# Kernel optimization log

Measured on AMD Instinct MI355X. Metric: run time of the kernel, lower is better.

## Reference

```python
import jax, jax.numpy as jnp
import numpy as np

N_NODES = 100000
N_EDGES = 3200000
D_IN = 256
D_HID = 32
N_CLS = 40
K_HOPS = 3


def setup_inputs() -> dict:
    key = jax.random.key(0)
    ks = jax.random.split(key, 6)
    x = jax.random.normal(ks[0], (N_NODES, D_IN), dtype=jnp.float32)
    edge_index = jax.random.randint(ks[1], (2, N_EDGES), 0, N_NODES, dtype=jnp.int64)
    edge_attr = jax.random.uniform(ks[2], (N_EDGES, 1), dtype=jnp.float32)
    W_conv = jax.random.normal(ks[3], (D_HID, D_IN), dtype=jnp.float32) / np.sqrt(D_IN)
    b_conv = jnp.zeros((D_HID,), dtype=jnp.float32)
    W_fc = jax.random.normal(ks[4], (N_CLS, D_HID), dtype=jnp.float32) * np.sqrt(2.0 / D_HID)
    b_fc = jnp.zeros((N_CLS,), dtype=jnp.float32)
    return {"x": x, "edge_index": edge_index, "edge_attr": edge_attr,
            "W_conv": W_conv, "b_conv": b_conv, "W_fc": W_fc, "b_fc": b_fc}


def _gcn_norm(edge_index, edge_weight, num_nodes):
    # add self-loops with weight 1 (PyG gcn_norm default)
    loop = jnp.arange(num_nodes, dtype=edge_index.dtype)
    row = jnp.concatenate([edge_index[0], loop])
    col = jnp.concatenate([edge_index[1], loop])
    w = jnp.concatenate([edge_weight, jnp.ones((num_nodes,), edge_weight.dtype)])
    deg = jax.ops.segment_sum(w, col, num_segments=num_nodes)
    deg_inv_sqrt = jnp.where(deg > 0, jax.lax.rsqrt(deg), 0.0)
    norm = deg_inv_sqrt[row] * w * deg_inv_sqrt[col]
    return row, col, norm


def reference(x, edge_index, edge_attr, W_conv, b_conv, W_fc, b_fc):
    N = x.shape[0]
    row, col, norm = _gcn_norm(edge_index, edge_attr.squeeze(-1), N)
    # K-hop symmetric-normalized diffusion: x <- (D^-1/2 (A+I) D^-1/2) x
    h = x
    for _ in range(K_HOPS):
        h = jax.ops.segment_sum(norm[:, None] * h[row], col, num_segments=N)
    h = h @ W_conv.T + b_conv          # SGConv linear
    h = jax.nn.elu(h)
    h = h @ W_fc.T + b_fc              # classifier
    return jax.nn.log_softmax(h, axis=1)
```

## Files before the change

kernel.cpp:

```cpp
#include <hip/hip_runtime.h>
#include <math.h>

#define N_NODES 100000
#define N_EDGES 3200000
#define D_IN    256
#define D_HID   32
#define N_CLS   40

#define NPART  196
#define HROW   200
#define NB1    256
#define CHUNK1 12500
#define SUB    2500

typedef unsigned int u32;
typedef unsigned short u16;

__device__ __forceinline__ float bf2f(u16 v) {
    return __uint_as_float(((u32)v) << 16);
}
__device__ __forceinline__ u16 f2bf(float f) {
    u32 u = __float_as_uint(f);
    u32 r = u + 0x7FFFu + ((u >> 16) & 1u);
    return (u16)(r >> 16);
}


__global__ __launch_bounds__(256) void k_histA(const int* __restrict__ col,
                                               u32* __restrict__ histmat) {
    __shared__ u32 h[256];
    int t = threadIdx.x;
    h[t] = 0;
    __syncthreads();
    int s = blockIdx.x * CHUNK1;
    for (int i = s + t; i < s + CHUNK1; i += 256)
        atomicAdd(&h[((u32)col[i]) >> 9], 1u);
    __syncthreads();
    if (t < HROW) histmat[blockIdx.x * HROW + t] = (t < NPART) ? h[t] : 0u;
}


__global__ __launch_bounds__(256) void k_scanA(u32* __restrict__ histmat,
                                               int* __restrict__ cstart) {
    __shared__ u32 sc[256];
    int p = threadIdx.x;
    u32 run = 0;
    for (int b = 0; b < NB1; ++b) {
        u32 v = (p < NPART) ? histmat[b * HROW + p] : 0u;
        if (p < NPART) histmat[b * HROW + p] = run;
        run += v;
    }
    u32 own = (p < NPART) ? run : 0u;
    sc[p] = own;
    __syncthreads();
    for (int off = 1; off < 256; off <<= 1) {
        u32 v = (p >= off) ? sc[p - off] : 0u;
        __syncthreads();
        sc[p] += v;
        __syncthreads();
    }
    if (p < NPART) cstart[p] = (int)(sc[p] - own);
    if (p == NPART - 1) cstart[NPART] = (int)sc[p];
}


__global__ __launch_bounds__(256) void k_part(const int* __restrict__ row,
                                              const int* __restrict__ col,
                                              const float* __restrict__ w,
                                              const u32* __restrict__ histmat,
                                              const int* __restrict__ cstart,
                                              uint2* __restrict__ coarse) {
    __shared__ u32 shist[256], sscan[256], scur[256], gbase[256], rcur[256];
    __shared__ uint2 stage[SUB];
    __shared__ u32 gdst[SUB];
    int t = threadIdx.x;
    rcur[t] = (t < NPART) ? ((u32)cstart[t] + histmat[blockIdx.x * HROW + t]) : 0u;
    int s0 = blockIdx.x * CHUNK1;

    for (int sc_ = 0; sc_ < CHUNK1; sc_ += SUB) {
        int s = s0 + sc_;
        shist[t] = 0;
        __syncthreads();
        for (int i = s + t; i < s + SUB; i += 256)
            atomicAdd(&shist[((u32)col[i]) >> 9], 1u);
        __syncthreads();
        u32 own = shist[t];
        sscan[t] = own;
        __syncthreads();
        for (int off = 1; off < 256; off <<= 1) {
            u32 v = (t >= off) ? sscan[t - off] : 0u;
            __syncthreads();
            sscan[t] += v;
            __syncthreads();
        }
        u32 exc = sscan[t] - own;
        scur[t]  = exc;
        gbase[t] = rcur[t] - exc;
        __syncthreads();
        for (int i = s + t; i < s + SUB; i += 256) {
            u32 c = (u32)col[i];
            u32 pid = c >> 9;
            u32 pos = atomicAdd(&scur[pid], 1u);
            stage[pos] = make_uint2(((c & 511u) << 17) | (u32)row[i], __float_as_uint(w[i]));
            gdst[pos]  = gbase[pid] + pos;
        }
        __syncthreads();
        for (int i = t; i < SUB; i += 256) coarse[gdst[i]] = stage[i];
        rcur[t] += shist[t];
        __syncthreads();
    }
}


__global__ __launch_bounds__(256) void k_part2(const uint2* __restrict__ coarse,
                                               const int* __restrict__ cstart,
                                               float* __restrict__ dis,
                                               int* __restrict__ startp,
                                               u32* __restrict__ csr) {
    __shared__ float wsuml[512];
    __shared__ u32 cntl[512];
    __shared__ u32 curl[512];
    __shared__ u32 psum[256];
    int p = blockIdx.x, t = threadIdx.x;
    int s = cstart[p], e = cstart[p + 1];
    int nbase = p << 9;

    cntl[t] = 0; cntl[t + 256] = 0;
    wsuml[t] = 0.f; wsuml[t + 256] = 0.f;
    __syncthreads();
    for (int i = s + t; i < e; i += 256) {
        uint2 en = coarse[i];
        u32 l = en.x >> 17;
        atomicAdd(&cntl[l], 1u);
        atomicAdd(&wsuml[l], __uint_as_float(en.y));
    }
    __syncthreads();
    for (int l = t; l < 512; l += 256) {
        int node = nbase + l;
        if (node < N_NODES) dis[node] = rsqrtf(1.0f + wsuml[l]);
    }
    u32 a0 = cntl[2 * t], a1 = cntl[2 * t + 1];
    psum[t] = a0 + a1;
    __syncthreads();
    for (int off = 1; off < 256; off <<= 1) {
        u32 v = (t >= off) ? psum[t - off] : 0u;
        __syncthreads();
        psum[t] += v;
        __syncthreads();
    }
    u32 excl = psum[t] - (a0 + a1);
    u32 c0 = (u32)s + excl, c1 = c0 + a0;
    curl[2 * t] = c0; curl[2 * t + 1] = c1;
    int n0 = nbase + 2 * t, n1 = n0 + 1;
    if (n0 < N_NODES) startp[n0] = (int)c0;
    if (n1 < N_NODES) startp[n1] = (int)c1;
    if (p == NPART - 1 && t == 255) startp[N_NODES] = e;
    __syncthreads();
    for (int i = s + t; i < e; i += 256) {
        uint2 en = coarse[i];
        u32 l = en.x >> 17;
        u32 src = en.x & 0x1FFFFu;
        float wv = __uint_as_float(en.y);
        u32 q = (u32)(wv * 32768.0f + 0.5f);
        if (q > 32767u) q = 32767u;
        u32 pos = atomicAdd(&curl[l], 1u);
        csr[pos] = (src << 15) | q;
    }
}


#define LSTRIDE 260

__global__ __launch_bounds__(256) void k_gemm1(const float* __restrict__ x,
                                               const float* __restrict__ Wc,
                                               const float* __restrict__ dis,
                                               u16* __restrict__ g) {
    __shared__ float xs[32 * LSTRIDE];
    __shared__ float wsl[32 * LSTRIDE];
    const int tid  = threadIdx.x;
    const int base = blockIdx.x * 32;

    for (int i = tid; i < 2048; i += 256) {
        int r = i >> 6, j = i & 63;
        float4 v = reinterpret_cast<const float4*>(x)[(size_t)(base + r) * 64 + j];
        *reinterpret_cast<float4*>(&xs[r * LSTRIDE + j * 4]) = v;
    }
    for (int i = tid; i < 2048; i += 256) {
        int r = i >> 6, j = i & 63;
        float4 v = reinterpret_cast<const float4*>(Wc)[i];
        *reinterpret_cast<float4*>(&wsl[r * LSTRIDE + j * 4]) = v;
    }
    __syncthreads();

    const int node = tid >> 3;
    const int og   = tid & 7;
    float4 acc = make_float4(0.f, 0.f, 0.f, 0.f);
    const float* xrow = &xs[node * LSTRIDE];
    const float* w0 = &wsl[(og     ) * LSTRIDE];
    const float* w1 = &wsl[(og +  8) * LSTRIDE];
    const float* w2 = &wsl[(og + 16) * LSTRIDE];
    const float* w3 = &wsl[(og + 24) * LSTRIDE];

#pragma unroll 4
    for (int k = 0; k < 256; k += 4) {
        float4 xv = *reinterpret_cast<const float4*>(&xrow[k]);
        float4 a4 = *reinterpret_cast<const float4*>(&w0[k]);
        float4 b4 = *reinterpret_cast<const float4*>(&w1[k]);
        float4 c4 = *reinterpret_cast<const float4*>(&w2[k]);
        float4 d4 = *reinterpret_cast<const float4*>(&w3[k]);
        acc.x += xv.x * a4.x + xv.y * a4.y + xv.z * a4.z + xv.w * a4.w;
        acc.y += xv.x * b4.x + xv.y * b4.y + xv.z * b4.z + xv.w * b4.w;
        acc.z += xv.x * c4.x + xv.y * c4.y + xv.z * c4.z + xv.w * c4.w;
        acc.w += xv.x * d4.x + xv.y * d4.y + xv.z * d4.z + xv.w * d4.w;
    }
    float dv = dis[base + node];
    size_t gb = (size_t)(base + node) * D_HID;
    g[gb + og     ] = f2bf(acc.x * dv);
    g[gb + og +  8] = f2bf(acc.y * dv);
    g[gb + og + 16] = f2bf(acc.z * dv);
    g[gb + og + 24] = f2bf(acc.w * dv);
}


__global__ __launch_bounds__(256) void k_pull(const int* __restrict__ start,
                                              const u32* __restrict__ csr,
                                              const float* __restrict__ dis,
                                              const u16* __restrict__ h,
                                              u16* __restrict__ out,
                                              int sq) {
    int g    = blockIdx.x * 8 + (threadIdx.x >> 5);
    int lane = threadIdx.x & 31;
    if (g >= N_NODES) return;

    int s = start[g];
    int e = start[g + 1];
    float acc = bf2f(h[(size_t)g * D_HID + lane]);

    for (int base = s; base < e; base += 32) {
        int idx = base + lane;
        u32 p = (idx < e) ? csr[idx] : 0u;
        int rem = e - base;
        for (int jj = 0; jj < 32; jj += 8) {
            if (jj >= rem) break;
#pragma unroll
            for (int j = 0; j < 8; ++j) {
                u32 pj = __shfl(p, jj + j, 32);
                float nv = (float)(pj & 32767u) * (1.0f / 32768.0f);
                u32 src = pj >> 15;
                acc += nv * bf2f(h[(size_t)src * D_HID + lane]);
            }
        }
    }
    float sc = dis[g];
    if (sq) sc *= sc;
    out[(size_t)g * D_HID + lane] = f2bf(sc * acc);
}


__global__ __launch_bounds__(256) void k_final(const u16* __restrict__ h,
                                               const float* __restrict__ bc,
                                               const float* __restrict__ Wfc,
                                               const float* __restrict__ bf,
                                               float* __restrict__ out) {
    __shared__ float wf[N_CLS * D_HID];
    __shared__ float bcs[D_HID];
    __shared__ float bfs[N_CLS];
    const int tid = threadIdx.x;
    for (int i = tid; i < N_CLS * D_HID; i += 256) wf[i] = Wfc[i];
    if (tid < D_HID) bcs[tid] = bc[tid];
    if (tid < N_CLS) bfs[tid] = bf[tid];
    __syncthreads();

    int node = blockIdx.x * 256 + tid;
    if (node >= N_NODES) return;

    float a[D_HID];
    const u32* hp = reinterpret_cast<const u32*>(h + (size_t)node * D_HID);
#pragma unroll
    for (int j = 0; j < 16; ++j) {
        u32 v = hp[j];
        float z0 = bf2f((u16)(v & 0xFFFFu)) + bcs[j * 2 + 0];
        float z1 = bf2f((u16)(v >> 16))     + bcs[j * 2 + 1];
        a[j * 2 + 0] = z0 > 0.f ? z0 : expm1f(z0);
        a[j * 2 + 1] = z1 > 0.f ? z1 : expm1f(z1);
    }

    float logits[N_CLS];
    float m = -1e30f;
#pragma unroll
    for (int c = 0; c < N_CLS; ++c) {
        float accv = bfs[c];
        const float* wr = &wf[c * D_HID];
#pragma unroll
        for (int o = 0; o < D_HID; ++o) accv += a[o] * wr[o];
        logits[c] = accv;
        m = fmaxf(m, accv);
    }
    float sum = 0.f;
#pragma unroll
    for (int c = 0; c < N_CLS; ++c) sum += expf(logits[c] - m);
    float lse = m + logf(sum);
    float* op = out + (size_t)node * N_CLS;
#pragma unroll
    for (int c = 0; c < N_CLS; ++c) op[c] = logits[c] - lse;
}


extern "C" void kernel_launch(void* const* d_in, const int* in_sizes, int n_in,
                              void* d_out, int out_size, void* d_ws, size_t ws_size,
                              hipStream_t stream) {
    const float* x   = (const float*)d_in[0];
    const int*   ei  = (const int*)d_in[1];
    const float* ea  = (const float*)d_in[2];
    const float* Wc  = (const float*)d_in[3];
    const float* bc  = (const float*)d_in[4];
    const float* Wfc = (const float*)d_in[5];
    const float* bf  = (const float*)d_in[6];
    float* out = (float*)d_out;
    float* ws  = (float*)d_ws;

    const int* row = ei;
    const int* col = ei + N_EDGES;

    float* dis     = ws;
    int*   cstart  = (int*)(ws + 100000);
    u32*   histmat = (u32*)(ws + 100224);
    int*   startp  = (int*)(ws + 151424);
    uint2* coarse  = (uint2*)(ws + 251428);
    u32*   csr     = (u32*)(ws + 6651428);
    u16*   bufA    = (u16*)(ws + 251428);
    u16*   bufB    = (u16*)(ws + 1851428);

    const int GN = (N_NODES + 255) / 256;
    const int GP = (N_NODES + 7) / 8;

    k_histA <<<NB1, 256, 0, stream>>>(col, histmat);
    k_scanA <<<1, 256, 0, stream>>>(histmat, cstart);
    k_part  <<<NB1, 256, 0, stream>>>(row, col, ea, histmat, cstart, coarse);
    k_part2 <<<NPART, 256, 0, stream>>>(coarse, cstart, dis, startp, csr);

    k_gemm1 <<<N_NODES / 32, 256, 0, stream>>>(x, Wc, dis, bufA);

    k_pull  <<<GP, 256, 0, stream>>>(startp, csr, dis, bufA, bufB, 1);
    k_pull  <<<GP, 256, 0, stream>>>(startp, csr, dis, bufB, bufA, 1);
    k_pull  <<<GP, 256, 0, stream>>>(startp, csr, dis, bufA, bufB, 0);

    k_final <<<GN, 256, 0, stream>>>(bufB, bc, Wfc, bf, out);
}
```

Baseline: 565.0 us.

## Use bf16 dot2 in projection GEMM and full-wavefront edge pulls

The projection GEMM now converts x and W to packed bf16 in shared memory, uses bf16 dot2 instructions, and computes two nodes per thread over 64-node blocks, which halves LDS traffic and raises reuse of the W loads. The pull kernel gives each node a full 64-lane wavefront: the two half-waves process alternate edges and their sums are combined with a cross-half shuffle, so the 32-wide wave32-style mapping no longer leaves half of each wave idle. The trade-offs are extra bf16 rounding of the inputs and fewer nodes handled per block in the pull kernel.

```diff
diff --git a/kernel.cpp b/kernel.cpp
--- a/kernel.cpp
+++ b/kernel.cpp
@@ -23,6 +23,30 @@
     u32 u = __float_as_uint(f);
     u32 r = u + 0x7FFFu + ((u >> 16) & 1u);
     return (u16)(r >> 16);
+}
+__device__ __forceinline__ u32 pack2bf(float lo, float hi) {
+    return (u32)f2bf(lo) | ((u32)f2bf(hi) << 16);
+}
+
+#if defined(__has_builtin)
+#if __has_builtin(__builtin_amdgcn_fdot2_f32_bf16)
+#define HAVE_DOT2 1
+#endif
+#endif
+
+#ifdef HAVE_DOT2
+typedef __bf16 bf16x2 __attribute__((ext_vector_type(2)));
+#endif
+
+__device__ __forceinline__ float dot2bf(u32 a, u32 b, float c) {
+#ifdef HAVE_DOT2
+    return __builtin_amdgcn_fdot2_f32_bf16(__builtin_bit_cast(bf16x2, a),
+                                           __builtin_bit_cast(bf16x2, b), c, false);
+#else
+    float al = __uint_as_float(a << 16), ah = __uint_as_float(a & 0xFFFF0000u);
+    float bl = __uint_as_float(b << 16), bh = __uint_as_float(b & 0xFFFF0000u);
+    return c + al * bl + ah * bh;
+#endif
 }
 
 
@@ -169,56 +193,77 @@
 }
 
 
-#define LSTRIDE 260
+#define XST 130
 
 __global__ __launch_bounds__(256) void k_gemm1(const float* __restrict__ x,
                                                const float* __restrict__ Wc,
                                                const float* __restrict__ dis,
                                                u16* __restrict__ g) {
-    __shared__ float xs[32 * LSTRIDE];
-    __shared__ float wsl[32 * LSTRIDE];
+    __shared__ u32 xs[64 * XST];
+    __shared__ u32 wsl[32 * XST];
     const int tid  = threadIdx.x;
-    const int base = blockIdx.x * 32;
-
-    for (int i = tid; i < 2048; i += 256) {
-        int r = i >> 6, j = i & 63;
-        float4 v = reinterpret_cast<const float4*>(x)[(size_t)(base + r) * 64 + j];
-        *reinterpret_cast<float4*>(&xs[r * LSTRIDE + j * 4]) = v;
-    }
-    for (int i = tid; i < 2048; i += 256) {
-        int r = i >> 6, j = i & 63;
-        float4 v = reinterpret_cast<const float4*>(Wc)[i];
-        *reinterpret_cast<float4*>(&wsl[r * LSTRIDE + j * 4]) = v;
-    }
-    __syncthreads();
-
-    const int node = tid >> 3;
-    const int og   = tid & 7;
-    float4 acc = make_float4(0.f, 0.f, 0.f, 0.f);
-    const float* xrow = &xs[node * LSTRIDE];
-    const float* w0 = &wsl[(og     ) * LSTRIDE];
-    const float* w1 = &wsl[(og +  8) * LSTRIDE];
-    const float* w2 = &wsl[(og + 16) * LSTRIDE];
-    const float* w3 = &wsl[(og + 24) * LSTRIDE];
+    const int base = blockIdx.x * 64;
+    const int nrows = (N_NODES - base) < 64 ? (N_NODES - base) : 64;
+
+    for (int i = tid; i < 4096; i += 256) {
+        int r = i >> 7, kk = i & 127;
+        float2 v = reinterpret_cast<const float2*>(Wc)[i];
+        wsl[r * XST + kk] = pack2bf(v.x, v.y);
+    }
+    for (int i = tid; i < nrows * 128; i += 256) {
+        int r = i >> 7, kk = i & 127;
+        float2 v = reinterpret_cast<const float2*>(x)[(size_t)(base + r) * 128 + kk];
+        xs[r * XST + kk] = pack2bf(v.x, v.y);
+    }
+    __syncthreads();
+
+    const int np = tid >> 3;
+    const int og = tid & 7;
+    if (2 * np >= nrows) return;
+
+    const u32* x0 = &xs[(2 * np    ) * XST];
+    const u32* x1 = &xs[(2 * np + 1) * XST];
+    const u32* w0 = &wsl[(og     ) * XST];
+    const u32* w1 = &wsl[(og +  8) * XST];
+    const u32* w2 = &wsl[(og + 16) * XST];
+    const u32* w3 = &wsl[(og + 24) * XST];
+
+    float a00 = 0.f, a01 = 0.f, a02 = 0.f, a03 = 0.f;
+    float a10 = 0.f, a11 = 0.f, a12 = 0.f, a13 = 0.f;
 
 #pragma unroll 4
-    for (int k = 0; k < 256; k += 4) {
-        float4 xv = *reinterpret_cast<const float4*>(&xrow[k]);
-        float4 a4 = *reinterpret_cast<const float4*>(&w0[k]);
-        float4 b4 = *reinterpret_cast<const float4*>(&w1[k]);
-        float4 c4 = *reinterpret_cast<const float4*>(&w2[k]);
-        float4 d4 = *reinterpret_cast<const float4*>(&w3[k]);
-        acc.x += xv.x * a4.x + xv.y * a4.y + xv.z * a4.z + xv.w * a4.w;
-        acc.y += xv.x * b4.x + xv.y * b4.y + xv.z * b4.z + xv.w * b4.w;
-        acc.z += xv.x * c4.x + xv.y * c4.y + xv.z * c4.z + xv.w * c4.w;
-        acc.w += xv.x * d4.x + xv.y * d4.y + xv.z * d4.z + xv.w * d4.w;
-    }
-    float dv = dis[base + node];
-    size_t gb = (size_t)(base + node) * D_HID;
-    g[gb + og     ] = f2bf(acc.x * dv);
-    g[gb + og +  8] = f2bf(acc.y * dv);
-    g[gb + og + 16] = f2bf(acc.z * dv);
-    g[gb + og + 24] = f2bf(acc.w * dv);
+    for (int kk = 0; kk < 128; kk += 2) {
+        uint2 X0 = *reinterpret_cast<const uint2*>(&x0[kk]);
+        uint2 X1 = *reinterpret_cast<const uint2*>(&x1[kk]);
+        uint2 W0 = *reinterpret_cast<const uint2*>(&w0[kk]);
+        uint2 W1 = *reinterpret_cast<const uint2*>(&w1[kk]);
+        uint2 W2 = *reinterpret_cast<const uint2*>(&w2[kk]);
+        uint2 W3 = *reinterpret_cast<const uint2*>(&w3[kk]);
+        a00 = dot2bf(X0.x, W0.x, a00); a00 = dot2bf(X0.y, W0.y, a00);
+        a01 = dot2bf(X0.x, W1.x, a01); a01 = dot2bf(X0.y, W1.y, a01);
+        a02 = dot2bf(X0.x, W2.x, a02); a02 = dot2bf(X0.y, W2.y, a02);
+        a03 = dot2bf(X0.x, W3.x, a03); a03 = dot2bf(X0.y, W3.y, a03);
+        a10 = dot2bf(X1.x, W0.x, a10); a10 = dot2bf(X1.y, W0.y, a10);
+        a11 = dot2bf(X1.x, W1.x, a11); a11 = dot2bf(X1.y, W1.y, a11);
+        a12 = dot2bf(X1.x, W2.x, a12); a12 = dot2bf(X1.y, W2.y, a12);
+        a13 = dot2bf(X1.x, W3.x, a13); a13 = dot2bf(X1.y, W3.y, a13);
+    }
+
+    int n0 = base + 2 * np;
+    float d0 = dis[n0];
+    size_t gb0 = (size_t)n0 * D_HID;
+    g[gb0 + og     ] = f2bf(a00 * d0);
+    g[gb0 + og +  8] = f2bf(a01 * d0);
+    g[gb0 + og + 16] = f2bf(a02 * d0);
+    g[gb0 + og + 24] = f2bf(a03 * d0);
+    if (2 * np + 1 < nrows) {
+        float d1 = dis[n0 + 1];
+        size_t gb1 = gb0 + D_HID;
+        g[gb1 + og     ] = f2bf(a10 * d1);
+        g[gb1 + og +  8] = f2bf(a11 * d1);
+        g[gb1 + og + 16] = f2bf(a12 * d1);
+        g[gb1 + og + 24] = f2bf(a13 * d1);
+    }
 }
 
 
@@ -228,32 +273,39 @@
                                               const u16* __restrict__ h,
                                               u16* __restrict__ out,
                                               int sq) {
-    int g    = blockIdx.x * 8 + (threadIdx.x >> 5);
-    int lane = threadIdx.x & 31;
-    if (g >= N_NODES) return;
-
-    int s = start[g];
-    int e = start[g + 1];
-    float acc = bf2f(h[(size_t)g * D_HID + lane]);
-
-    for (int base = s; base < e; base += 32) {
-        int idx = base + lane;
+    int wid  = blockIdx.x * 4 + (threadIdx.x >> 6);
+    int lane = threadIdx.x & 63;
+    int dim  = lane & 31;
+    if (wid >= N_NODES) return;
+
+    int s = start[wid];
+    int e = start[wid + 1];
+    float acc = 0.f;
+
+    for (int base = s; base < e; base += 64) {
+        int idx = base + 2 * dim + (lane >> 5);
         u32 p = (idx < e) ? csr[idx] : 0u;
         int rem = e - base;
-        for (int jj = 0; jj < 32; jj += 8) {
-            if (jj >= rem) break;
+        int npairs = (rem + 1) >> 1;
+        if (npairs > 32) npairs = 32;
+        for (int j0 = 0; j0 < 32; j0 += 8) {
+            if (j0 >= npairs) break;
 #pragma unroll
             for (int j = 0; j < 8; ++j) {
-                u32 pj = __shfl(p, jj + j, 32);
+                u32 pj = __shfl(p, j0 + j + (lane & 32), 64);
                 float nv = (float)(pj & 32767u) * (1.0f / 32768.0f);
                 u32 src = pj >> 15;
-                acc += nv * bf2f(h[(size_t)src * D_HID + lane]);
+                acc += nv * bf2f(h[(size_t)src * D_HID + dim]);
             }
         }
     }
-    float sc = dis[g];
-    if (sq) sc *= sc;
-    out[(size_t)g * D_HID + lane] = f2bf(sc * acc);
+    float tot = acc + __shfl_xor(acc, 32, 64);
+    if (lane < 32) {
+        tot += bf2f(h[(size_t)wid * D_HID + dim]);
+        float sc = dis[wid];
+        if (sq) sc *= sc;
+        out[(size_t)wid * D_HID + dim] = f2bf(sc * tot);
+    }
 }
 
 
@@ -332,14 +384,15 @@
     u16*   bufB    = (u16*)(ws + 1851428);
 
     const int GN = (N_NODES + 255) / 256;
-    const int GP = (N_NODES + 7) / 8;
+    const int GG = (N_NODES + 63) / 64;
+    const int GP = (N_NODES + 3) / 4;
 
     k_histA <<<NB1, 256, 0, stream>>>(col, histmat);
     k_scanA <<<1, 256, 0, stream>>>(histmat, cstart);
     k_part  <<<NB1, 256, 0, stream>>>(row, col, ea, histmat, cstart, coarse);
     k_part2 <<<NPART, 256, 0, stream>>>(coarse, cstart, dis, startp, csr);
 
-    k_gemm1 <<<N_NODES / 32, 256, 0, stream>>>(x, Wc, dis, bufA);
+    k_gemm1 <<<GG, 256, 0, stream>>>(x, Wc, dis, bufA);
 
     k_pull  <<<GP, 256, 0, stream>>>(startp, csr, dis, bufA, bufB, 1);
     k_pull  <<<GP, 256, 0, stream>>>(startp, csr, dis, bufB, bufA, 1);
```

After: 561.7 us. No clear change (-0.6%).
